# Performance work log

Measured on AMD Instinct MI355X. Metric: run time of the kernel, lower is better.

Reference implementation:

```python
import jax, jax.numpy as jnp
import numpy as np

J = 15       # joints
D = 128      # per-joint feature dim
ANG = 3      # per-joint angle dim
EPS = 1e-12  # F.normalize eps
TEMP = 200.0
SCALE = 16.0


def setup_inputs() -> dict:
    key = jax.random.key(0)
    k1, k2 = jax.random.split(key)
    B, N, E = 16384, 68, J * D + J * ANG  # E = 1965
    emb = jax.random.normal(k1, (B, E), dtype=jnp.float32)
    W = jax.random.normal(k2, (N, E), dtype=jnp.float32)
    return {"emb": emb, "W": W}


def reference(emb, W):
    B = emb.shape[0]
    N = W.shape[0]
    # split feature / angle blocks
    x_feat = emb[:, : J * D].reshape(B, J, D)        # (B, 15, 128)
    x_ang = emb[:, J * D :].reshape(B, 1, J, ANG)    # (B, 1, 15, 3)
    p_feat = W[:, : J * D].reshape(N, J, D)          # (N, 15, 128)
    p_ang = W[:, J * D :].reshape(1, N, J, ANG)      # (1, N, 15, 3)

    # per-joint angle distance and (detached in torch) softmax weighting
    ang_w = jnp.linalg.norm(x_ang - p_ang, axis=-1)            # (B, N, 15)
    w2 = jax.nn.softmax(ang_w / TEMP, axis=-1) * J             # (B, N, 15)

    # NOTE: the torch code computes argsort(ang_w) but immediately overwrites the
    # index with an identity permutation (ind = [0..14]), so the gather is a no-op.
    # Hence normalization is over the flat 15*128 block per batch / per class.
    xn = x_feat / jnp.maximum(
        jnp.linalg.norm(x_feat.reshape(B, -1), axis=-1), EPS
    )[:, None, None]
    pn = p_feat / jnp.maximum(
        jnp.linalg.norm(p_feat.reshape(N, -1), axis=-1), EPS
    )[:, None, None]

    # per-joint cosine contributions, weighted and summed
    s = jnp.einsum("bjd,njd->bnj", xn, pn)                     # (B, N, 15)
    logit = (s * w2).sum(-1) * SCALE                           # (B, N)
    return logit
```

## Files before the change

### kernel.cpp

```cpp
#include <hip/hip_runtime.h>
#include <hip/hip_bf16.h>

typedef __bf16 bf16x8 __attribute__((ext_vector_type(8)));
typedef __bf16 bf16x4 __attribute__((ext_vector_type(4)));
typedef float  f32x4  __attribute__((ext_vector_type(4)));

static constexpr int E    = 1965;
static constexpr int KF   = 1920;
static constexpr int NJ   = 15;
static constexpr int NCLS = 68;
static constexpr int NPAD = 80;
static constexpr int NT   = 5;
static constexpr int NS   = 60;
static constexpr int AST  = 1928;

static constexpr size_t PNF_BYTES = (size_t)NT * NS * 64 * 8 * 2;

__global__ __launch_bounds__(256) void prep_kernel(const float* __restrict__ W,
                                                   __bf16* __restrict__ pnf,
                                                   float* __restrict__ pa) {
    const int n = blockIdx.x;
    const int t = threadIdx.x;
    float v[8];
    float ss = 0.f;
    if (n < NCLS && t < 240) {
        const float* src = W + (size_t)n * E + 8 * t;
        #pragma unroll
        for (int i = 0; i < 8; ++i) { v[i] = src[i]; ss += v[i] * v[i]; }
    } else {
        #pragma unroll
        for (int i = 0; i < 8; ++i) v[i] = 0.f;
    }
    #pragma unroll
    for (int off = 32; off >= 1; off >>= 1) ss += __shfl_xor(ss, off);
    __shared__ float rbuf[4];
    if ((t & 63) == 0) rbuf[t >> 6] = ss;
    __syncthreads();
    const float total = rbuf[0] + rbuf[1] + rbuf[2] + rbuf[3];
    const float rnorm = 1.f / fmaxf(sqrtf(total), 1e-12f);

    if (t < 240) {
        bf16x8 o;
        #pragma unroll
        for (int i = 0; i < 8; ++i) o[i] = (__bf16)(v[i] * rnorm);
        const int s = t >> 2, g = t & 3;
        const int lane = (n & 15) + 16 * g;
        const size_t off = (((size_t)(n >> 4) * NS + s) * 64 + lane) * 8;
        *(bf16x8*)(pnf + off) = o;
    }
    if (t < 45) {
        pa[n * 45 + t] = (n < NCLS) ? W[(size_t)n * E + KF + t] : 0.f;
    }
}

__global__ __launch_bounds__(320) void cos_kernel(const float* __restrict__ emb,
                                                  const __bf16* __restrict__ pnf,
                                                  const float* __restrict__ pa,
                                                  float* __restrict__ out) {
    __shared__ __bf16 A[16][AST];
    __shared__ __bf16 pal[NPAD][52];
    __shared__ float  xa[16][48];
    __shared__ float  sp[320];
    __shared__ float  srow[16];

    const int tid = threadIdx.x;
    const int m0  = blockIdx.x * 16;

    for (int idx = tid; idx < 16 * 45; idx += 320) {
        const int r = idx / 45, c = idx - r * 45;
        xa[r][c] = emb[(size_t)(m0 + r) * E + KF + c];
    }
    for (int idx = tid; idx < NPAD * 45; idx += 320) {
        const int n = idx / 45, c = idx - n * 45;
        pal[n][c] = (__bf16)pa[idx];
    }

    const int row = tid / 20;
    const int sc  = tid % 20;
    const float* arow = emb + (size_t)(m0 + row) * E + 4 * sc;
    f32x4 av[24];
    #pragma unroll
    for (int i = 0; i < 24; ++i)
        __builtin_memcpy(&av[i], arow + 80 * i, 16);

    float ssq = 0.f;
    #pragma unroll
    for (int i = 0; i < 24; ++i) {
        bf16x4 o;
        #pragma unroll
        for (int q = 0; q < 4; ++q) {
            const float x = av[i][q];
            ssq += x * x;
            o[q] = (__bf16)x;
        }
        *(bf16x4*)&A[row][4 * sc + 80 * i] = o;
    }
    sp[tid] = ssq;
    __syncthreads();

    if (tid < 16) {
        float s = 0.f;
        #pragma unroll
        for (int i = 0; i < 20; ++i) s += sp[tid * 20 + i];
        srow[tid] = s;
    }

    const int w  = tid >> 6;
    const int l  = tid & 63;
    const int lr = l & 15;
    const int lg = l >> 4;
    const bf16x8* bp = (const bf16x8*)pnf + (size_t)w * NS * 64 + l;
    const __bf16* ab = &A[lr][0];

    f32x4 acc[NJ];
    #pragma unroll
    for (int j = 0; j < NJ; ++j) acc[j] = f32x4{0.f, 0.f, 0.f, 0.f};

    #pragma unroll
    for (int s = 0; s < NS; ++s) {
        const bf16x8 b = bp[s * 64];
        const bf16x8 a = *(const bf16x8*)(ab + 32 * s + 8 * lg);
        acc[s >> 2] = __builtin_amdgcn_mfma_f32_16x16x32_bf16(a, b, acc[s >> 2], 0, 0, 0);
    }
    __syncthreads();

    const int r0  = lg * 4;
    const int col = w * 16 + lr;

    float rn[4];
    #pragma unroll
    for (int r = 0; r < 4; ++r)
        rn[r] = 240.f / fmaxf(sqrtf(srow[r0 + r]), 1e-12f);

    float pr[45];
    #pragma unroll
    for (int q = 0; q < 12; ++q) {
        const bf16x4 pv = *(const bf16x4*)&pal[col][4 * q];
        #pragma unroll
        for (int e = 0; e < 4; ++e)
            if (4 * q + e < 45) pr[4 * q + e] = (float)pv[e];
    }

    float num[4] = {0.f, 0.f, 0.f, 0.f};
    float den[4] = {0.f, 0.f, 0.f, 0.f};
    #pragma unroll
    for (int r = 0; r < 4; ++r) {
        f32x4 xr[12];
        #pragma unroll
        for (int q = 0; q < 12; ++q)
            xr[q] = *(const f32x4*)&xa[r0 + r][4 * q];
        #pragma unroll
        for (int j = 0; j < NJ; ++j) {
            const float d0 = xr[(3 * j + 0) >> 2][(3 * j + 0) & 3] - pr[3 * j + 0];
            const float d1 = xr[(3 * j + 1) >> 2][(3 * j + 1) & 3] - pr[3 * j + 1];
            const float d2 = xr[(3 * j + 2) >> 2][(3 * j + 2) & 3] - pr[3 * j + 2];
            const float dist = sqrtf(d0 * d0 + d1 * d1 + d2 * d2);
            const float e = __expf(dist * 0.005f);
            den[r] += e;
            num[r] += e * acc[j][r];
        }
    }

    if (col < NCLS) {
        #pragma unroll
        for (int r = 0; r < 4; ++r)
            out[(size_t)(m0 + r0 + r) * NCLS + col] = rn[r] * num[r] / den[r];
    }
}

extern "C" void kernel_launch(void* const* d_in, const int* in_sizes, int n_in,
                              void* d_out, int out_size, void* d_ws, size_t ws_size,
                              hipStream_t stream) {
    const float* emb = (const float*)d_in[0];
    const float* W   = (const float*)d_in[1];
    float* out = (float*)d_out;
    __bf16* pnf = (__bf16*)d_ws;
    float*  pa  = (float*)((char*)d_ws + PNF_BYTES);
    const int B = in_sizes[0] / E;

    prep_kernel<<<NPAD, 256, 0, stream>>>(W, pnf, pa);
    cos_kernel<<<B / 16, 320, 0, stream>>>(emb, pnf, pa, out);
}
```

Before: 72.92 us.

## Stream emb rows into double-buffered LDS via global_load_lds and compute norms in-wave

Replaces the up-front load, convert and store of the whole 16x1920 emb tile into bf16 LDS with a 6-chunk double-buffered pipeline. It uses direct global-to-LDS loads of fp32 data, and conversion to bf16 happens just before each MFMA. Each wave now computes the row sum of squares from the fragments it reads and reduces them with shuffles, which removes the shared partial-sum array and one block barrier. The goal is to overlap global memory latency with MFMA work and shrink the LDS footprint so occupancy can rise. The cost is two barriers per chunk and redundant fp32-to-bf16 conversion and squaring in every wave.

Result: slower. 84.63 us (+16.1%).

```diff
diff --git a/kernel.cpp b/kernel.cpp
--- a/kernel.cpp
+++ b/kernel.cpp
@@ -12,7 +12,11 @@
 static constexpr int NPAD = 80;
 static constexpr int NT   = 5;
 static constexpr int NS   = 60;
-static constexpr int AST  = 1928;
+
+static constexpr int CH   = 6;
+static constexpr int CCOL = 320;
+static constexpr int CST  = 10;
+static constexpr int SEGS = 80;
 
 static constexpr size_t PNF_BYTES = (size_t)NT * NS * 64 * 8 * 2;
 
@@ -57,14 +61,16 @@
                                                   const __bf16* __restrict__ pnf,
                                                   const float* __restrict__ pa,
                                                   float* __restrict__ out) {
-    __shared__ __bf16 A[16][AST];
+    __shared__ f32x4  Abuf[2][SEGS][16];
     __shared__ __bf16 pal[NPAD][52];
     __shared__ float  xa[16][48];
-    __shared__ float  sp[320];
-    __shared__ float  srow[16];
 
     const int tid = threadIdx.x;
     const int m0  = blockIdx.x * 16;
+    const int w   = tid >> 6;
+    const int l   = tid & 63;
+    const int lr  = l & 15;
+    const int lg  = l >> 4;
 
     for (int idx = tid; idx < 16 * 45; idx += 320) {
         const int r = idx / 45, c = idx - r * 45;
@@ -74,55 +80,64 @@
         const int n = idx / 45, c = idx - n * 45;
         pal[n][c] = (__bf16)pa[idx];
     }
+    asm volatile("s_waitcnt lgkmcnt(0)" ::: "memory");
 
-    const int row = tid / 20;
-    const int sc  = tid % 20;
-    const float* arow = emb + (size_t)(m0 + row) * E + 4 * sc;
-    f32x4 av[24];
-    #pragma unroll
-    for (int i = 0; i < 24; ++i)
-        __builtin_memcpy(&av[i], arow + 80 * i, 16);
+    const float* gbase = emb + (size_t)(m0 + lr) * E + (16 * w + lg) * 4;
+    #define ISSUE_CHUNK(c)                                                              \
+        {                                                                               \
+            const float* g_ = gbase + (c) * CCOL;                                       \
+            _Pragma("unroll")                                                           \
+            for (int i_ = 0; i_ < 4; ++i_)                                              \
+                __builtin_amdgcn_global_load_lds(                                       \
+                    (const __attribute__((address_space(1))) void*)(g_ + i_ * 16),      \
+                    (__attribute__((address_space(3))) void*)&Abuf[(c) & 1][16 * w + 4 * i_][0], \
+                    16, 0, 0);                                                          \
+        }
 
-    float ssq = 0.f;
-    #pragma unroll
-    for (int i = 0; i < 24; ++i) {
-        bf16x4 o;
-        #pragma unroll
-        for (int q = 0; q < 4; ++q) {
-            const float x = av[i][q];
-            ssq += x * x;
-            o[q] = (__bf16)x;
-        }
-        *(bf16x4*)&A[row][4 * sc + 80 * i] = o;
-    }
-    sp[tid] = ssq;
-    __syncthreads();
+    ISSUE_CHUNK(0);
 
-    if (tid < 16) {
-        float s = 0.f;
-        #pragma unroll
-        for (int i = 0; i < 20; ++i) s += sp[tid * 20 + i];
-        srow[tid] = s;
-    }
-
-    const int w  = tid >> 6;
-    const int l  = tid & 63;
-    const int lr = l & 15;
-    const int lg = l >> 4;
     const bf16x8* bp = (const bf16x8*)pnf + (size_t)w * NS * 64 + l;
-    const __bf16* ab = &A[lr][0];
 
     f32x4 acc[NJ];
     #pragma unroll
     for (int j = 0; j < NJ; ++j) acc[j] = f32x4{0.f, 0.f, 0.f, 0.f};
+    float ssq = 0.f;
 
     #pragma unroll
-    for (int s = 0; s < NS; ++s) {
-        const bf16x8 b = bp[s * 64];
-        const bf16x8 a = *(const bf16x8*)(ab + 32 * s + 8 * lg);
-        acc[s >> 2] = __builtin_amdgcn_mfma_f32_16x16x32_bf16(a, b, acc[s >> 2], 0, 0, 0);
+    for (int c = 0; c < CH; ++c) {
+        __builtin_amdgcn_s_barrier();
+        if (c + 1 < CH) {
+            ISSUE_CHUNK(c + 1);
+            asm volatile("s_waitcnt vmcnt(4)" ::: "memory");
+        } else {
+            asm volatile("s_waitcnt vmcnt(0)" ::: "memory");
+        }
+        __builtin_amdgcn_s_barrier();
+
+        bf16x8 bfr[CST];
+        #pragma unroll
+        for (int s = 0; s < CST; ++s) bfr[s] = bp[(c * CST + s) * 64];
+
+        #pragma unroll
+        for (int s = 0; s < CST; ++s) {
+            const f32x4 alo = Abuf[c & 1][8 * s + 2 * lg][lr];
+            const f32x4 ahi = Abuf[c & 1][8 * s + 2 * lg + 1][lr];
+            bf16x8 af;
+            #pragma unroll
+            for (int q = 0; q < 4; ++q) {
+                ssq += alo[q] * alo[q];
+                ssq += ahi[q] * ahi[q];
+                af[q]     = (__bf16)alo[q];
+                af[4 + q] = (__bf16)ahi[q];
+            }
+            acc[(c * CST + s) >> 2] =
+                __builtin_amdgcn_mfma_f32_16x16x32_bf16(af, bfr[s], acc[(c * CST + s) >> 2], 0, 0, 0);
+        }
     }
-    __syncthreads();
+    #undef ISSUE_CHUNK
+
+    ssq += __shfl_xor(ssq, 16);
+    ssq += __shfl_xor(ssq, 32);
 
     const int r0  = lg * 4;
     const int col = w * 16 + lr;
@@ -130,7 +145,7 @@
     float rn[4];
     #pragma unroll
     for (int r = 0; r < 4; ++r)
-        rn[r] = 240.f / fmaxf(sqrtf(srow[r0 + r]), 1e-12f);
+        rn[r] = 240.f / fmaxf(sqrtf(__shfl(ssq, r0 + r)), 1e-12f);
 
     float pr[45];
     #pragma unroll
```
